# Optimization experiments

Hardware: AMD Instinct MI355X
Metric: run time of the kernel (lower is better)

## Reference

```python
import jax, jax.numpy as jnp
import numpy as np


def setup_inputs() -> dict:
    key = jax.random.key(0)
    k1, k2, k3 = jax.random.split(key, 3)
    B, D, T, DEPTH = 16384, 512, 64, 6
    x = jax.random.normal(k1, (B, D), dtype=jnp.float32)
    # per-tree learned params, stacked over the tree axis (num_trees)
    feature_selectors = jax.random.normal(k2, (T, DEPTH, D), dtype=jnp.float32)
    thresholds = jnp.zeros((T, DEPTH), dtype=jnp.float32)
    leaf_weights = jax.random.normal(k3, (T, 2 ** DEPTH, 1), dtype=jnp.float32)
    return {"x": x, "feature_selectors": feature_selectors,
            "thresholds": thresholds, "leaf_weights": leaf_weights}


def reference(x, feature_selectors, thresholds, leaf_weights):
    # x: [B, D]; feature_selectors: [T, depth, D]; thresholds: [T, depth]
    # leaf_weights: [T, 2^depth, 1]
    B = x.shape[0]
    T, depth, _ = feature_selectors.shape
    # all trees' split logits in one GEMM: [B, T, depth]
    logits = jnp.einsum('bi,tdi->btd', x, feature_selectors) - thresholds
    probs = jax.nn.sigmoid(logits)
    # probs_stack[..., 0] = p, probs_stack[..., 1] = 1 - p  -> [B, T, depth, 2]
    probs_stack = jnp.stack([probs, 1.0 - probs], axis=-1)
    # build leaf probabilities via repeated outer products over the depth axis
    leaf = probs_stack[:, :, 0]  # [B, T, 2]
    for d in range(1, depth):
        # [B, T, 2^d, 1] * [B, T, 1, 2] -> [B, T, 2^(d+1)]
        leaf = (leaf[..., :, None] * probs_stack[:, :, d][:, :, None, :]).reshape(B, T, -1)
    # per-tree leaf_probs @ weights, summed over trees -> [B, 1]
    out = jnp.einsum('btl,tlo->bo', leaf, leaf_weights)
    return out
```

## Files before the change

kernel.cpp:

```cpp
#include <hip/hip_runtime.h>


#define DD     512
#define NCOL   384
#define PKELT  (NCOL * DD)
#define XSTR   520
#define PRSTR  388

typedef __bf16 bf16_t;
typedef __bf16 bf16x8 __attribute__((ext_vector_type(8)));
typedef float  f32x4  __attribute__((ext_vector_type(4)));

static __device__ __forceinline__ float b2f(unsigned int u16) {
  unsigned int t = u16 << 16;
  float f;
  __builtin_memcpy(&f, &t, 4);
  return f;
}

static __device__ __forceinline__ float fast_sigmoid(float z) {
  float e = __builtin_amdgcn_exp2f(z * -1.44269504f);
  return __builtin_amdgcn_rcpf(1.0f + e);
}

__global__ __launch_bounds__(256) void node_prep(const float* __restrict__ fsel,
                                                 const float* __restrict__ x,
                                                 bf16_t* __restrict__ pk,
                                                 bf16_t* __restrict__ xbf)
{
  if (blockIdx.x < 96) {
    int tid  = blockIdx.x * 256 + threadIdx.x;
    int lane = tid & 63;
    int ksg  = (tid >> 6) & 15;
    int cf   = tid >> 10;
    int col  = cf * 16 + (lane & 15);
    int k    = ksg * 32 + (lane >> 4) * 8;
    float4 f0 = *reinterpret_cast<const float4*>(fsel + (size_t)col * DD + k);
    float4 f1 = *reinterpret_cast<const float4*>(fsel + (size_t)col * DD + k + 4);
    bf16x8 v;
    v[0] = (bf16_t)f0.x; v[1] = (bf16_t)f0.y; v[2] = (bf16_t)f0.z; v[3] = (bf16_t)f0.w;
    v[4] = (bf16_t)f1.x; v[5] = (bf16_t)f1.y; v[6] = (bf16_t)f1.z; v[7] = (bf16_t)f1.w;
    #pragma unroll
    for (int c = 0; c < 8; ++c)
      *reinterpret_cast<bf16x8*>(pk + (size_t)c * PKELT + (size_t)tid * 8) = v;
  } else {
    size_t idx = (size_t)(blockIdx.x - 96) * 256 + threadIdx.x;
    size_t e   = idx * 8;
    float4 f0 = *reinterpret_cast<const float4*>(x + e);
    float4 f1 = *reinterpret_cast<const float4*>(x + e + 4);
    bf16x8 v;
    v[0] = (bf16_t)f0.x; v[1] = (bf16_t)f0.y; v[2] = (bf16_t)f0.z; v[3] = (bf16_t)f0.w;
    v[4] = (bf16_t)f1.x; v[5] = (bf16_t)f1.y; v[6] = (bf16_t)f1.z; v[7] = (bf16_t)f1.w;
    *reinterpret_cast<bf16x8*>(xbf + e) = v;
  }
}

__global__ __launch_bounds__(512, 2) void node_fused(
    const bf16_t* __restrict__ xbf,
    const bf16_t* __restrict__ pk,
    const float*  __restrict__ thr,
    const float*  __restrict__ lw,
    float*        __restrict__ out)
{
  __shared__ bf16_t xs[64 * XSTR];
  __shared__ bf16_t pr[64 * PRSTR];

  const int tid  = threadIdx.x;
  const int lane = tid & 63;
  const int wv   = tid >> 6;
  const int rowblk = blockIdx.x * 64;
  const int c   = lane & 15;
  const int kg  = lane >> 4;

  float th[3];
  #pragma unroll
  for (int f = 0; f < 3; ++f) th[f] = thr[wv * 48 + f * 16 + c];

  #pragma unroll
  for (int i = 0; i < 8; ++i) {
    const int row = wv * 8 + i;
    __builtin_amdgcn_global_load_lds(
        (const __attribute__((address_space(1))) unsigned int*)(const void*)
            (xbf + (size_t)(rowblk + row) * DD + lane * 8),
        (__attribute__((address_space(3))) unsigned int*)(void*)
            (&xs[row * XSTR]),
        16, 0, 0);
  }

  bf16x8 bhA[3][2], bhB[3][2];
  #define LOAD_BH(B_, n)                                                        \
    do {                                                                        \
      const bf16_t* q_ = pk + (size_t)(blockIdx.x & 7) * PKELT +                \
                         (size_t)lane * 8 + (size_t)(n) * 1024 +                \
                         (size_t)wv * 3 * 8192;                                 \
      asm volatile("" : "+v"(q_));                                              \
      _Pragma("unroll")                                                         \
      for (int f_ = 0; f_ < 3; ++f_)                                            \
        _Pragma("unroll")                                                       \
        for (int ks_ = 0; ks_ < 2; ++ks_)                                       \
          B_[f_][ks_] = *reinterpret_cast<const bf16x8*>(q_ + f_ * 8192 + ks_ * 512); \
    } while (0)

  asm volatile("s_waitcnt vmcnt(0)" ::: "memory");
  __builtin_amdgcn_s_barrier();

  LOAD_BH(bhA, 0);
  LOAD_BH(bhB, 1);

  f32x4 acc[4][3];
  #pragma unroll
  for (int t = 0; t < 4; ++t)
    #pragma unroll
    for (int f = 0; f < 3; ++f) acc[t][f] = (f32x4){0.f, 0.f, 0.f, 0.f};

  #define CHUNK(ch, CUR)                                                        \
    do {                                                                        \
      _Pragma("unroll")                                                         \
      for (int t = 0; t < 4; ++t) {                                             \
        _Pragma("unroll")                                                       \
        for (int ks = 0; ks < 2; ++ks) {                                        \
          bf16x8 a = *reinterpret_cast<const bf16x8*>(                          \
              &xs[(t * 16 + c) * XSTR + (ch) * 64 + ks * 32 + kg * 8]);         \
          acc[t][0] = __builtin_amdgcn_mfma_f32_16x16x32_bf16(a, CUR[0][ks], acc[t][0], 0, 0, 0); \
          acc[t][1] = __builtin_amdgcn_mfma_f32_16x16x32_bf16(a, CUR[1][ks], acc[t][1], 0, 0, 0); \
          acc[t][2] = __builtin_amdgcn_mfma_f32_16x16x32_bf16(a, CUR[2][ks], acc[t][2], 0, 0, 0); \
        }                                                                       \
      }                                                                         \
      if ((ch) + 2 < 8) LOAD_BH(CUR, (ch) + 2);                                 \
    } while (0)

  CHUNK(0, bhA);
  CHUNK(1, bhB);
  CHUNK(2, bhA);
  CHUNK(3, bhB);
  CHUNK(4, bhA);
  CHUNK(5, bhB);
  CHUNK(6, bhA);
  CHUNK(7, bhB);
  #undef CHUNK
  #undef LOAD_BH

  #pragma unroll
  for (int t = 0; t < 4; ++t) {
    #pragma unroll
    for (int f = 0; f < 3; ++f) {
      const int col = wv * 48 + f * 16 + c;
      #pragma unroll
      for (int r = 0; r < 4; ++r) {
        const int row = t * 16 + kg * 4 + r;
        pr[row * PRSTR + col] = (bf16_t)fast_sigmoid(acc[t][f][r] - th[f]);
      }
    }
  }
  asm volatile("s_waitcnt lgkmcnt(0)" ::: "memory");
  __builtin_amdgcn_s_barrier();

  float p0v[8], hv0[8], hv1[8];
  #pragma unroll
  for (int half = 0; half < 2; ++half) {
    float wch[32];
    #pragma unroll
    for (int j = 0; j < 8; ++j) {
      float4 f4 = *reinterpret_cast<const float4*>(lw + (size_t)lane * 64 + half * 32 + j * 4);
      wch[4*j] = f4.x; wch[4*j+1] = f4.y; wch[4*j+2] = f4.z; wch[4*j+3] = f4.w;
    }
    #pragma unroll
    for (int rr = 0; rr < 8; ++rr) {
      const int row = wv * 8 + rr;
      const unsigned int* prow =
          reinterpret_cast<const unsigned int*>(&pr[row * PRSTR]) + lane * 3;
      unsigned int d0 = prow[0], d1 = prow[1], d2 = prow[2];
      float p1 = b2f(d0 >> 16);
      float p2 = b2f(d1 & 0xffffu), p3 = b2f(d1 >> 16);
      float p4 = b2f(d2 & 0xffffu), p5 = b2f(d2 >> 16);
      if (half == 0) p0v[rr] = b2f(d0 & 0xffffu);

      float v[16];
      #pragma unroll
      for (int j = 0; j < 16; ++j) v[j] = fmaf(p5, wch[2*j] - wch[2*j+1], wch[2*j+1]);
      #pragma unroll
      for (int j = 0; j < 8;  ++j) v[j] = fmaf(p4, v[2*j] - v[2*j+1], v[2*j+1]);
      #pragma unroll
      for (int j = 0; j < 4;  ++j) v[j] = fmaf(p3, v[2*j] - v[2*j+1], v[2*j+1]);
      #pragma unroll
      for (int j = 0; j < 2;  ++j) v[j] = fmaf(p2, v[2*j] - v[2*j+1], v[2*j+1]);
      float s = fmaf(p1, v[0] - v[1], v[1]);
      if (half == 0) hv0[rr] = s; else hv1[rr] = s;
    }
  }

  float tvv[8];
  #pragma unroll
  for (int rr = 0; rr < 8; ++rr)
    tvv[rr] = fmaf(p0v[rr], hv0[rr] - hv1[rr], hv1[rr]);

  #pragma unroll
  for (int off = 32; off; off >>= 1) {
    #pragma unroll
    for (int rr = 0; rr < 8; ++rr) tvv[rr] += __shfl_xor(tvv[rr], off, 64);
  }
  if (lane == 0) {
    #pragma unroll
    for (int rr = 0; rr < 8; ++rr) out[rowblk + wv * 8 + rr] = tvv[rr];
  }
}

extern "C" void kernel_launch(void* const* d_in, const int* in_sizes, int n_in,
                              void* d_out, int out_size, void* d_ws, size_t ws_size,
                              hipStream_t stream) {
  const float* x    = (const float*)d_in[0];
  const float* fsel = (const float*)d_in[1];
  const float* thr  = (const float*)d_in[2];
  const float* lw   = (const float*)d_in[3];
  float* out = (float*)d_out;

  char* ws = (char*)d_ws;
  bf16_t* pk  = (bf16_t*)ws;
  bf16_t* xbf = (bf16_t*)(ws + 8 * 393216);

  const int B = in_sizes[0] / DD;

  node_prep<<<dim3(96 + (B * DD / 8 / 256)), dim3(256), 0, stream>>>(fsel, x, pk, xbf);
  node_fused<<<dim3(B / 64), dim3(512), 0, stream>>>(xbf, pk, thr, lw, out);
}
```

Measured before the change: 30.65 us.

## Fuse x bf16 conversion into main kernel and use 1024-thread blocks

Drops the separate x-to-bf16 pass and its workspace round-trip: the fused kernel now loads fp32 x directly, converts it in registers and writes bf16 into LDS. Blocks grow to 1024 threads (16 waves) split into 2 row groups by 8 column groups, so each wave handles half the rows and the leaf stage does 4 rows per wave. This removes one full read and write of x in bf16. In exchange the fused kernel reads fp32 x (twice the bytes) through registers instead of the async global-to-LDS load, and the larger blocks may lower occupancy.

```diff
diff --git a/kernel.cpp b/kernel.cpp
--- a/kernel.cpp
+++ b/kernel.cpp
@@ -9,6 +9,7 @@
 
 typedef __bf16 bf16_t;
 typedef __bf16 bf16x8 __attribute__((ext_vector_type(8)));
+typedef __bf16 bf16x4 __attribute__((ext_vector_type(4)));
 typedef float  f32x4  __attribute__((ext_vector_type(4)));
 
 static __device__ __forceinline__ float b2f(unsigned int u16) {
@@ -23,40 +24,27 @@
   return __builtin_amdgcn_rcpf(1.0f + e);
 }
 
-__global__ __launch_bounds__(256) void node_prep(const float* __restrict__ fsel,
-                                                 const float* __restrict__ x,
-                                                 bf16_t* __restrict__ pk,
-                                                 bf16_t* __restrict__ xbf)
+__global__ __launch_bounds__(256) void node_pack(const float* __restrict__ fsel,
+                                                 bf16_t* __restrict__ pk)
 {
-  if (blockIdx.x < 96) {
-    int tid  = blockIdx.x * 256 + threadIdx.x;
-    int lane = tid & 63;
-    int ksg  = (tid >> 6) & 15;
-    int cf   = tid >> 10;
-    int col  = cf * 16 + (lane & 15);
-    int k    = ksg * 32 + (lane >> 4) * 8;
-    float4 f0 = *reinterpret_cast<const float4*>(fsel + (size_t)col * DD + k);
-    float4 f1 = *reinterpret_cast<const float4*>(fsel + (size_t)col * DD + k + 4);
-    bf16x8 v;
-    v[0] = (bf16_t)f0.x; v[1] = (bf16_t)f0.y; v[2] = (bf16_t)f0.z; v[3] = (bf16_t)f0.w;
-    v[4] = (bf16_t)f1.x; v[5] = (bf16_t)f1.y; v[6] = (bf16_t)f1.z; v[7] = (bf16_t)f1.w;
-    #pragma unroll
-    for (int c = 0; c < 8; ++c)
-      *reinterpret_cast<bf16x8*>(pk + (size_t)c * PKELT + (size_t)tid * 8) = v;
-  } else {
-    size_t idx = (size_t)(blockIdx.x - 96) * 256 + threadIdx.x;
-    size_t e   = idx * 8;
-    float4 f0 = *reinterpret_cast<const float4*>(x + e);
-    float4 f1 = *reinterpret_cast<const float4*>(x + e + 4);
-    bf16x8 v;
-    v[0] = (bf16_t)f0.x; v[1] = (bf16_t)f0.y; v[2] = (bf16_t)f0.z; v[3] = (bf16_t)f0.w;
-    v[4] = (bf16_t)f1.x; v[5] = (bf16_t)f1.y; v[6] = (bf16_t)f1.z; v[7] = (bf16_t)f1.w;
-    *reinterpret_cast<bf16x8*>(xbf + e) = v;
-  }
-}
-
-__global__ __launch_bounds__(512, 2) void node_fused(
-    const bf16_t* __restrict__ xbf,
+  int tid  = blockIdx.x * 256 + threadIdx.x;
+  int lane = tid & 63;
+  int ksg  = (tid >> 6) & 15;
+  int cf   = tid >> 10;
+  int col  = cf * 16 + (lane & 15);
+  int k    = ksg * 32 + (lane >> 4) * 8;
+  float4 f0 = *reinterpret_cast<const float4*>(fsel + (size_t)col * DD + k);
+  float4 f1 = *reinterpret_cast<const float4*>(fsel + (size_t)col * DD + k + 4);
+  bf16x8 v;
+  v[0] = (bf16_t)f0.x; v[1] = (bf16_t)f0.y; v[2] = (bf16_t)f0.z; v[3] = (bf16_t)f0.w;
+  v[4] = (bf16_t)f1.x; v[5] = (bf16_t)f1.y; v[6] = (bf16_t)f1.z; v[7] = (bf16_t)f1.w;
+  #pragma unroll
+  for (int c = 0; c < 8; ++c)
+    *reinterpret_cast<bf16x8*>(pk + (size_t)c * PKELT + (size_t)tid * 8) = v;
+}
+
+__global__ __launch_bounds__(1024) void node_fused(
+    const float*  __restrict__ x,
     const bf16_t* __restrict__ pk,
     const float*  __restrict__ thr,
     const float*  __restrict__ lw,
@@ -68,23 +56,21 @@
   const int tid  = threadIdx.x;
   const int lane = tid & 63;
   const int wv   = tid >> 6;
+  const int wr   = wv >> 3;
+  const int wc   = wv & 7;
   const int rowblk = blockIdx.x * 64;
   const int c   = lane & 15;
   const int kg  = lane >> 4;
 
   float th[3];
   #pragma unroll
-  for (int f = 0; f < 3; ++f) th[f] = thr[wv * 48 + f * 16 + c];
-
+  for (int f = 0; f < 3; ++f) th[f] = thr[wc * 48 + f * 16 + c];
+
+  float4 st[8];
   #pragma unroll
   for (int i = 0; i < 8; ++i) {
-    const int row = wv * 8 + i;
-    __builtin_amdgcn_global_load_lds(
-        (const __attribute__((address_space(1))) unsigned int*)(const void*)
-            (xbf + (size_t)(rowblk + row) * DD + lane * 8),
-        (__attribute__((address_space(3))) unsigned int*)(void*)
-            (&xs[row * XSTR]),
-        16, 0, 0);
+    int idx = i * 1024 + tid, e = idx << 2, r = e >> 9, k = e & 511;
+    st[i] = *reinterpret_cast<const float4*>(x + (size_t)(rowblk + r) * DD + k);
   }
 
   bf16x8 bhA[3][2], bhB[3][2];
@@ -92,7 +78,7 @@
     do {                                                                        \
       const bf16_t* q_ = pk + (size_t)(blockIdx.x & 7) * PKELT +                \
                          (size_t)lane * 8 + (size_t)(n) * 1024 +                \
-                         (size_t)wv * 3 * 8192;                                 \
+                         (size_t)wc * 3 * 8192;                                 \
       asm volatile("" : "+v"(q_));                                              \
       _Pragma("unroll")                                                         \
       for (int f_ = 0; f_ < 3; ++f_)                                            \
@@ -101,26 +87,34 @@
           B_[f_][ks_] = *reinterpret_cast<const bf16x8*>(q_ + f_ * 8192 + ks_ * 512); \
     } while (0)
 
-  asm volatile("s_waitcnt vmcnt(0)" ::: "memory");
-  __builtin_amdgcn_s_barrier();
-
   LOAD_BH(bhA, 0);
   LOAD_BH(bhB, 1);
 
-  f32x4 acc[4][3];
-  #pragma unroll
-  for (int t = 0; t < 4; ++t)
+  #pragma unroll
+  for (int i = 0; i < 8; ++i) {
+    int idx = i * 1024 + tid, e = idx << 2, r = e >> 9, k = e & 511;
+    bf16x4 v;
+    v[0] = (bf16_t)st[i].x; v[1] = (bf16_t)st[i].y;
+    v[2] = (bf16_t)st[i].z; v[3] = (bf16_t)st[i].w;
+    *reinterpret_cast<bf16x4*>(&xs[r * XSTR + k]) = v;
+  }
+  asm volatile("s_waitcnt lgkmcnt(0)" ::: "memory");
+  __builtin_amdgcn_s_barrier();
+
+  f32x4 acc[2][3];
+  #pragma unroll
+  for (int t = 0; t < 2; ++t)
     #pragma unroll
     for (int f = 0; f < 3; ++f) acc[t][f] = (f32x4){0.f, 0.f, 0.f, 0.f};
 
   #define CHUNK(ch, CUR)                                                        \
     do {                                                                        \
       _Pragma("unroll")                                                         \
-      for (int t = 0; t < 4; ++t) {                                             \
+      for (int t = 0; t < 2; ++t) {                                             \
         _Pragma("unroll")                                                       \
         for (int ks = 0; ks < 2; ++ks) {                                        \
           bf16x8 a = *reinterpret_cast<const bf16x8*>(                          \
-              &xs[(t * 16 + c) * XSTR + (ch) * 64 + ks * 32 + kg * 8]);         \
+              &xs[((wr * 2 + t) * 16 + c) * XSTR + (ch) * 64 + ks * 32 + kg * 8]); \
           acc[t][0] = __builtin_amdgcn_mfma_f32_16x16x32_bf16(a, CUR[0][ks], acc[t][0], 0, 0, 0); \
           acc[t][1] = __builtin_amdgcn_mfma_f32_16x16x32_bf16(a, CUR[1][ks], acc[t][1], 0, 0, 0); \
           acc[t][2] = __builtin_amdgcn_mfma_f32_16x16x32_bf16(a, CUR[2][ks], acc[t][2], 0, 0, 0); \
@@ -141,13 +135,13 @@
   #undef LOAD_BH
 
   #pragma unroll
-  for (int t = 0; t < 4; ++t) {
+  for (int t = 0; t < 2; ++t) {
     #pragma unroll
     for (int f = 0; f < 3; ++f) {
-      const int col = wv * 48 + f * 16 + c;
+      const int col = wc * 48 + f * 16 + c;
       #pragma unroll
       for (int r = 0; r < 4; ++r) {
-        const int row = t * 16 + kg * 4 + r;
+        const int row = (wr * 2 + t) * 16 + kg * 4 + r;
         pr[row * PRSTR + col] = (bf16_t)fast_sigmoid(acc[t][f][r] - th[f]);
       }
     }
@@ -155,7 +149,7 @@
   asm volatile("s_waitcnt lgkmcnt(0)" ::: "memory");
   __builtin_amdgcn_s_barrier();
 
-  float p0v[8], hv0[8], hv1[8];
+  float p0v[4], hv0[4], hv1[4];
   #pragma unroll
   for (int half = 0; half < 2; ++half) {
     float wch[32];
@@ -165,8 +159,8 @@
       wch[4*j] = f4.x; wch[4*j+1] = f4.y; wch[4*j+2] = f4.z; wch[4*j+3] = f4.w;
     }
     #pragma unroll
-    for (int rr = 0; rr < 8; ++rr) {
-      const int row = wv * 8 + rr;
+    for (int rr = 0; rr < 4; ++rr) {
+      const int row = wv * 4 + rr;
       const unsigned int* prow =
           reinterpret_cast<const unsigned int*>(&pr[row * PRSTR]) + lane * 3;
       unsigned int d0 = prow[0], d1 = prow[1], d2 = prow[2];
@@ -189,19 +183,19 @@
     }
   }
 
-  float tvv[8];
-  #pragma unroll
-  for (int rr = 0; rr < 8; ++rr)
+  float tvv[4];
+  #pragma unroll
+  for (int rr = 0; rr < 4; ++rr)
     tvv[rr] = fmaf(p0v[rr], hv0[rr] - hv1[rr], hv1[rr]);
 
   #pragma unroll
   for (int off = 32; off; off >>= 1) {
     #pragma unroll
-    for (int rr = 0; rr < 8; ++rr) tvv[rr] += __shfl_xor(tvv[rr], off, 64);
+    for (int rr = 0; rr < 4; ++rr) tvv[rr] += __shfl_xor(tvv[rr], off, 64);
   }
   if (lane == 0) {
     #pragma unroll
-    for (int rr = 0; rr < 8; ++rr) out[rowblk + wv * 8 + rr] = tvv[rr];
+    for (int rr = 0; rr < 4; ++rr) out[rowblk + wv * 4 + rr] = tvv[rr];
   }
 }
 
@@ -214,12 +208,10 @@
   const float* lw   = (const float*)d_in[3];
   float* out = (float*)d_out;
 
-  char* ws = (char*)d_ws;
-  bf16_t* pk  = (bf16_t*)ws;
-  bf16_t* xbf = (bf16_t*)(ws + 8 * 393216);
+  bf16_t* pk = (bf16_t*)d_ws;
 
   const int B = in_sizes[0] / DD;
 
-  node_prep<<<dim3(96 + (B * DD / 8 / 256)), dim3(256), 0, stream>>>(fsel, x, pk, xbf);
-  node_fused<<<dim3(B / 64), dim3(512), 0, stream>>>(xbf, pk, thr, lw, out);
-}
+  node_pack<<<dim3(96), dim3(256), 0, stream>>>(fsel, pk);
+  node_fused<<<dim3(B / 64), dim3(1024), 0, stream>>>(x, pk, thr, lw, out);
+}
```

Result: slower. 34.56 us (+12.8%).
